# Optimization experiments

Hardware: AMD Instinct MI355X
Metric: run time of the kernel (lower is better)

The kernel has to match this reference:

```python
import jax, jax.numpy as jnp
import numpy as np

S, B, H, D, IN = 512, 8, 8, 64, 512  # seq, batch, heads, head dim, model dim
PROJ = H * (5 * D + 2)


def setup_inputs() -> dict:
    key = jax.random.key(0)
    k0, k1, k2 = jax.random.split(key, 3)
    x = jax.random.normal(k0, (S, B, IN), jnp.float32)
    W_slow = jax.random.normal(k1, (PROJ, IN), jnp.float32) / np.sqrt(IN).astype(np.float32)
    W_out = jax.random.normal(k2, (IN, H * D), jnp.float32) / np.sqrt(H * D).astype(np.float32)
    ln_gamma = jnp.ones((IN,), jnp.float32)
    ln_beta = jnp.zeros((IN,), jnp.float32)
    return dict(x=x, W_slow=W_slow, W_out=W_out, ln_gamma=ln_gamma, ln_beta=ln_beta)


def reference(x, W_slow, W_out, ln_gamma, ln_beta):
    slen, bsz, in_dim = x.shape
    # pre-LayerNorm (torch LayerNorm: biased variance, eps=1e-5)
    mu = x.mean(-1, keepdims=True)
    var = x.var(-1, keepdims=True)
    normed = (x - mu) / jnp.sqrt(var + 1e-5) * ln_gamma + ln_beta
    qkvb = (normed @ W_slow.T).reshape(slen, bsz, H, 5 * D + 2)
    q, k, v, rk, rv, beta, rbeta = jnp.split(
        qkvb, [D, 2 * D, 3 * D, 4 * D, 5 * D, 5 * D + 1], axis=-1)
    q = jax.nn.softmax(q, axis=-1)
    k = jax.nn.softmax(k, axis=-1)
    rk = jax.nn.softmax(rk, axis=-1)
    beta = jax.nn.sigmoid(beta)    # (S,B,H,1)
    rbeta = jax.nn.sigmoid(rbeta)  # (S,B,H,1)

    # ---- fast_weight_memory: delta-rule fast weight, z_t = W_t q_t ----
    W0 = jnp.zeros((bsz, H, D, D), x.dtype)

    def fw_step(W, inp):
        qt, kt, vt, bt = inp  # (B,H,D),(B,H,D),(B,H,D),(B,H,1)
        v_old = jnp.einsum('bhij,bhj->bhi', W, kt)
        W = W + (bt * (vt - v_old))[..., :, None] * kt[..., None, :]
        z = jnp.einsum('bhij,bhj->bhi', W, qt)
        return W, z

    _, z = jax.lax.scan(fw_step, W0, (q, k, v, beta))  # z: (S,B,H,D)

    # ---- fast_rnn_v2: recurrent fast weight, h_t = z_t + R_t softmax(h_{t-1}) ----
    R0 = jnp.zeros((bsz, H, D, D), x.dtype)
    h0 = jnp.zeros((bsz, H, D), x.dtype)

    def rec_step(carry, inp):
        R, h = carry
        zt, kt, vt, bt = inp
        qh = jax.nn.softmax(h, axis=-1)
        v_old = jnp.einsum('bhij,bhj->bhi', R, kt)
        R = R + (bt * (vt - v_old))[..., :, None] * kt[..., None, :]
        h = zt + jnp.einsum('bhij,bhj->bhi', R, qh)
        return (R, h), h

    _, hs = jax.lax.scan(rec_step, (R0, h0), (z, rk, rv, rbeta))  # (S,B,H,D)

    out = hs.reshape(slen, bsz, H * D) @ W_out.T  # (S,B,IN)
    # dropout = 0.0 -> identity; residual
    return x + out
```

## Files before the change

### kernel.cpp

```cpp
#include <hip/hip_runtime.h>

#define S_LEN 512
#define BSZ 8
#define NH 8
#define HD 64
#define IN_DIM 512
#define PROJ 2576
#define SEG 322
#define AST 352
#define CHUNK 8
#define NCH 64
#define CB (CHUNK * AST * 4)

typedef __attribute__((ext_vector_type(8))) __bf16 bf16x8;
typedef __attribute__((ext_vector_type(4))) float f32x4;

static __device__ __forceinline__ unsigned short f2bf(float f) {
  unsigned u = __float_as_uint(f);
  unsigned r = (u + 0x7fffu + ((u >> 16) & 1u)) >> 16;
  return (unsigned short)r;
}
static __device__ __forceinline__ float bf2f(unsigned short s) {
  return __uint_as_float(((unsigned)s) << 16);
}

static __device__ __forceinline__ void gl_lds16(const void* g, void* l) {
  __builtin_amdgcn_global_load_lds(
      (const __attribute__((address_space(1))) unsigned int*)g,
      (__attribute__((address_space(3))) unsigned int*)l, 16, 0, 0);
}

static __device__ __forceinline__ void barrier_lgkm() {
  asm volatile("s_waitcnt lgkmcnt(0)" ::: "memory");
  __builtin_amdgcn_s_barrier();
  asm volatile("" ::: "memory");
}

__global__ __launch_bounds__(256) void ln_kernel(const float* __restrict__ x,
                                                 const float* __restrict__ gamma,
                                                 const float* __restrict__ beta,
                                                 unsigned short* __restrict__ out) {
  int wave = threadIdx.x >> 6, lane = threadIdx.x & 63;
  int row = blockIdx.x * 4 + wave;
  const float* xr = x + (size_t)row * IN_DIM + lane * 8;
  float4 a = *(const float4*)xr;
  float4 b = *(const float4*)(xr + 4);
  float vals[8] = {a.x, a.y, a.z, a.w, b.x, b.y, b.z, b.w};
  float s = 0.f, ss = 0.f;
#pragma unroll
  for (int i = 0; i < 8; i++) { s += vals[i]; ss += vals[i] * vals[i]; }
#pragma unroll
  for (int o = 32; o; o >>= 1) { s += __shfl_xor(s, o); ss += __shfl_xor(ss, o); }
  float mu = s * (1.f / 512.f);
  float var = ss * (1.f / 512.f) - mu * mu;
  float rstd = rsqrtf(var + 1e-5f);
  const float* g = gamma + lane * 8;
  const float* be = beta + lane * 8;
  float4 g1 = *(const float4*)g, g2 = *(const float4*)(g + 4);
  float4 b1 = *(const float4*)be, b2 = *(const float4*)(be + 4);
  float gs[8] = {g1.x, g1.y, g1.z, g1.w, g2.x, g2.y, g2.z, g2.w};
  float bs[8] = {b1.x, b1.y, b1.z, b1.w, b2.x, b2.y, b2.z, b2.w};
  union { unsigned short u[8]; uint4 v; } pk;
#pragma unroll
  for (int i = 0; i < 8; i++) pk.u[i] = f2bf((vals[i] - mu) * rstd * gs[i] + bs[i]);
  *(uint4*)(out + (size_t)row * IN_DIM + lane * 8) = pk.v;
}

__global__ void cast_kernel(const float* __restrict__ in, unsigned short* __restrict__ out, int n) {
  int i = blockIdx.x * blockDim.x + threadIdx.x;
  int st = gridDim.x * blockDim.x;
  for (; i < n; i += st) out[i] = f2bf(in[i]);
}

template <int BF16_OUT, int RESID>
__global__ __launch_bounds__(256) void gemm_bt(const unsigned short* __restrict__ A,
                                               const unsigned short* __restrict__ B,
                                               void* __restrict__ Cout,
                                               const float* __restrict__ resid,
                                               int M, int N, int K) {
  __shared__ __align__(16) unsigned short As[64][40];
  __shared__ __align__(16) unsigned short Bs[64][40];
  int tid = threadIdx.x;
  int lane = tid & 63, wave = tid >> 6;
  int m0 = blockIdx.y * 64, n0 = blockIdx.x * 64;
  int srow = tid >> 2, skq = (tid & 3) * 8;
  const unsigned short* Ap = A + (size_t)(m0 + srow) * K + skq;
  const unsigned short* Bp = B + (size_t)(n0 + srow) * K + skq;
  bool bvalid = (n0 + srow) < N;
  f32x4 zero = {0.f, 0.f, 0.f, 0.f};
  f32x4 acc[4];
#pragma unroll
  for (int nt = 0; nt < 4; nt++) acc[nt] = zero;
  int q = lane >> 4, m16 = lane & 15;
  for (int k0 = 0; k0 < K; k0 += 32) {
    uint4 av = *(const uint4*)(Ap + k0);
    uint4 bz = {0u, 0u, 0u, 0u};
    uint4 bv = bvalid ? *(const uint4*)(Bp + k0) : bz;
    *(uint4*)&As[srow][skq] = av;
    *(uint4*)&Bs[srow][skq] = bv;
    __syncthreads();
    bf16x8 af = *(const bf16x8*)&As[wave * 16 + m16][q * 8];
#pragma unroll
    for (int nt = 0; nt < 4; nt++) {
      bf16x8 bfv = *(const bf16x8*)&Bs[nt * 16 + m16][q * 8];
      acc[nt] = __builtin_amdgcn_mfma_f32_16x16x32_bf16(af, bfv, acc[nt], 0, 0, 0);
    }
    __syncthreads();
  }
  int rbase = q * 4;
#pragma unroll
  for (int nt = 0; nt < 4; nt++) {
#pragma unroll
    for (int rr = 0; rr < 4; rr++) {
      int gm = m0 + wave * 16 + rbase + rr;
      int gn = n0 + nt * 16 + m16;
      if (gn < N) {
        float v = acc[nt][rr];
        if (BF16_OUT) {
          ((unsigned short*)Cout)[(size_t)gm * N + gn] = f2bf(v);
        } else {
          float o = v;
          if (RESID) o += resid[(size_t)gm * N + gn];
          ((float*)Cout)[(size_t)gm * N + gn] = o;
        }
      }
    }
  }
}

__global__ __launch_bounds__(256) void act_kernel(const unsigned short* __restrict__ qkvb,
                                                  float* __restrict__ act) {
  int gw = blockIdx.x * 4 + (threadIdx.x >> 6);
  int l = threadIdx.x & 63;
  int m = gw >> 3, hh = gw & 7;
  int t = m >> 3, b = m & 7;
  const unsigned short* src = qkvb + (size_t)m * PROJ + hh * SEG;
  float fq = bf2f(src[l]);
  float fk = bf2f(src[64 + l]);
  float fv = bf2f(src[128 + l]);
  float fr = bf2f(src[192 + l]);
  float frv = bf2f(src[256 + l]);
  float mq = fq, mk = fk, mr = fr;
#pragma unroll
  for (int o = 32; o; o >>= 1) {
    mq = fmaxf(mq, __shfl_xor(mq, o));
    mk = fmaxf(mk, __shfl_xor(mk, o));
    mr = fmaxf(mr, __shfl_xor(mr, o));
  }
  float eq = __expf(fq - mq), ek = __expf(fk - mk), er = __expf(fr - mr);
  float sq = eq, sk = ek, sr = er;
#pragma unroll
  for (int o = 32; o; o >>= 1) {
    sq += __shfl_xor(sq, o);
    sk += __shfl_xor(sk, o);
    sr += __shfl_xor(sr, o);
  }
  int bh = b * 8 + hh;
  float* dst = act + ((size_t)bh * S_LEN + t) * AST;
  dst[l] = eq * __builtin_amdgcn_rcpf(sq);
  dst[64 + l] = ek * __builtin_amdgcn_rcpf(sk);
  dst[128 + l] = er * __builtin_amdgcn_rcpf(sr);
  dst[192 + l] = fv;
  dst[256 + l] = frv;
  if (l < 2) {
    float xv = bf2f(src[320 + l]);
    dst[320 + l] = __builtin_amdgcn_rcpf(1.f + __expf(-xv));
  }
}

__global__ __launch_bounds__(128, 1) void scan_kernel(const float* __restrict__ act,
                                                      unsigned short* __restrict__ hs) {
  int bh = blockIdx.x;
  int b = bh >> 3, hh = bh & 7;
  int tid = threadIdx.x, l = tid & 63, w = tid >> 6;

  __shared__ __align__(16) float stage[2][CHUNK * AST];
  __shared__ __align__(16) float zbuf[2][64];
  __shared__ __align__(16) float ehb[64];

  const char* abase = (const char*)(act + (size_t)bh * S_LEN * AST);

#pragma unroll
  for (int i = 0; i < 6; i++) {
    int idx = i * 2 + w;
    if (idx < 11)
      gl_lds16(abase + (size_t)idx * 1024 + l * 16, (char*)&stage[0][0] + idx * 1024);
  }
  if (w) ehb[l] = 1.f;

  f32x4 M[16];
#pragma unroll
  for (int j = 0; j < 16; j++) M[j] = (f32x4){0.f, 0.f, 0.f, 0.f};

  unsigned short* hdst = hs + (size_t)b * 512 + hh * 64 + l;

  asm volatile("s_waitcnt vmcnt(0) lgkmcnt(0)" ::: "memory");
  __builtin_amdgcn_s_barrier();
  asm volatile("" ::: "memory");

  for (int c = 0; c < NCH; c++) {
    int buf = c & 1;
    if (c + 1 < NCH) {
      const char* nb = abase + (size_t)(c + 1) * CB;
#pragma unroll
      for (int i = 0; i < 6; i++) {
        int idx = i * 2 + w;
        if (idx < 11)
          gl_lds16(nb + (size_t)idx * 1024 + l * 16, (char*)&stage[buf ^ 1][0] + idx * 1024);
      }
    }

    for (int s = 0; s < CHUNK; s++) {
      const float* stf = &stage[buf][s * AST];
      const f32x4* st4 = (const f32x4*)stf;
      int p = s & 1;
      f32x4 z4 = {0.f, 0.f, 0.f, 0.f};

      if (w == 0) {
        float cv = stf[192 + l];
        f32x4 kk[16];
#pragma unroll
        for (int j = 0; j < 16; j++) kk[j] = st4[16 + j];
        f32x4 a0 = z4, a1 = z4, a2 = z4, a3 = z4;
#pragma unroll
        for (int j = 0; j < 16; j += 4) {
          a0 += M[j] * kk[j];
          a1 += M[j + 1] * kk[j + 1];
          a2 += M[j + 2] * kk[j + 2];
          a3 += M[j + 3] * kk[j + 3];
        }
        f32x4 vo = (a0 + a1) + (a2 + a3);
        float vold = (vo.x + vo.y) + (vo.z + vo.w);
        float bt = stf[320];
        float coef = bt * (cv - vold);
        f32x4 c4 = {coef, coef, coef, coef};
        a0 = a1 = a2 = a3 = z4;
#pragma unroll
        for (int j = 0; j < 16; j += 4) {
          M[j] += c4 * kk[j];         a0 += M[j] * st4[j];
          M[j + 1] += c4 * kk[j + 1]; a1 += M[j + 1] * st4[j + 1];
          M[j + 2] += c4 * kk[j + 2]; a2 += M[j + 2] * st4[j + 2];
          M[j + 3] += c4 * kk[j + 3]; a3 += M[j + 3] * st4[j + 3];
        }
        vo = (a0 + a1) + (a2 + a3);
        zbuf[p][l] = (vo.x + vo.y) + (vo.z + vo.w);
        barrier_lgkm();
      } else {
        float cv = stf[256 + l];
        f32x4 kk[16];
#pragma unroll
        for (int j = 0; j < 16; j++) kk[j] = st4[32 + j];
        f32x4 a0 = z4, a1 = z4, a2 = z4, a3 = z4;
#pragma unroll
        for (int j = 0; j < 16; j += 4) {
          a0 += M[j] * kk[j];
          a1 += M[j + 1] * kk[j + 1];
          a2 += M[j + 2] * kk[j + 2];
          a3 += M[j + 3] * kk[j + 3];
        }
        f32x4 vo = (a0 + a1) + (a2 + a3);
        float rvold = (vo.x + vo.y) + (vo.z + vo.w);
        float rb = stf[321];
        float coef = rb * (cv - rvold);
        f32x4 c4 = {coef, coef, coef, coef};
        const f32x4* e4 = (const f32x4*)ehb;
        f32x4 s0 = z4, s1 = z4, s2v = z4, s3 = z4;
        a0 = a1 = a2 = a3 = z4;
#pragma unroll
        for (int j = 0; j < 16; j += 4) {
          f32x4 e0 = e4[j], e1 = e4[j + 1], e2 = e4[j + 2], e3 = e4[j + 3];
          M[j] += c4 * kk[j];         a0 += M[j] * e0;       s0 += e0;
          M[j + 1] += c4 * kk[j + 1]; a1 += M[j + 1] * e1;   s1 += e1;
          M[j + 2] += c4 * kk[j + 2]; a2 += M[j + 2] * e2;   s2v += e2;
          M[j + 3] += c4 * kk[j + 3]; a3 += M[j + 3] * e3;   s3 += e3;
        }
        f32x4 ho = (a0 + a1) + (a2 + a3);
        f32x4 so = (s0 + s1) + (s2v + s3);
        float hp = (ho.x + ho.y) + (ho.z + ho.w);
        float sm = (so.x + so.y) + (so.z + so.w);
        barrier_lgkm();
        float z = zbuf[p][l];
        float h = z + hp * __builtin_amdgcn_rcpf(sm);
        hdst[(size_t)(c * CHUNK + s) * (BSZ * 512)] = f2bf(h);
        ehb[l] = __expf(h - 20.f);
      }
    }

    if (c + 1 < NCH) {
      if (w == 0) {
        asm volatile("s_waitcnt vmcnt(0)" ::: "memory");
      } else {
        asm volatile("s_waitcnt vmcnt(8)" ::: "memory");
      }
      __builtin_amdgcn_s_barrier();
      asm volatile("" ::: "memory");
    }
  }
}

extern "C" void kernel_launch(void* const* d_in, const int* in_sizes, int n_in,
                              void* d_out, int out_size, void* d_ws, size_t ws_size,
                              hipStream_t stream) {
  const float* x = (const float*)d_in[0];
  const float* W_slow = (const float*)d_in[1];
  const float* W_out = (const float*)d_in[2];
  const float* gamma = (const float*)d_in[3];
  const float* beta = (const float*)d_in[4];

  char* ws = (char*)d_ws;
  size_t off = 0;
  unsigned short* normed = (unsigned short*)(ws + off); off += (size_t)4096 * 512 * 2;
  unsigned short* Wslow_b = (unsigned short*)(ws + off); off += (size_t)PROJ * 512 * 2;
  unsigned short* Wout_b = (unsigned short*)(ws + off); off += (size_t)512 * 512 * 2;
  unsigned short* qkvb = (unsigned short*)(ws + off); off += (size_t)4096 * PROJ * 2;
  float* act = (float*)(ws + off); off += (size_t)64 * S_LEN * AST * 4;
  unsigned short* hsb = normed;

  hipLaunchKernelGGL(ln_kernel, dim3(1024), dim3(256), 0, stream, x, gamma, beta, normed);
  hipLaunchKernelGGL(cast_kernel, dim3(512), dim3(256), 0, stream, W_slow, Wslow_b, PROJ * 512);
  hipLaunchKernelGGL(cast_kernel, dim3(256), dim3(256), 0, stream, W_out, Wout_b, 512 * 512);
  hipLaunchKernelGGL((gemm_bt<1, 0>), dim3((PROJ + 63) / 64, 4096 / 64), dim3(256), 0, stream,
                     normed, Wslow_b, (void*)qkvb, (const float*)nullptr, 4096, PROJ, 512);
  hipLaunchKernelGGL(act_kernel, dim3(8192), dim3(256), 0, stream, qkvb, act);
  hipLaunchKernelGGL(scan_kernel, dim3(64), dim3(128), 0, stream, act, hsb);
  hipLaunchKernelGGL((gemm_bt<0, 1>), dim3(512 / 64, 4096 / 64), dim3(256), 0, stream,
                     hsb, Wout_b, d_out, x, 4096, 512, 512);
}
```

Baseline: 480.4 us.

## Fuse fast-weight matvecs via rank-1 identity and use packed FP32 FMAs

Each scan step now computes the old-state matvecs against the key and the query (or the softmax vector) together in one pass. The contribution of the rank-1 update is added algebraically as coef*(k·q), with the dot product built by a wave shuffle reduction. The M update is moved after the barrier, which takes it off the cross-wave critical path. Register math switches to v_pk_fma_f32 on float2 pairs, and the softmax normaliser is a shuffle sum instead of an LDS loop. The explicit initialisation of the shared ehb buffer was removed, so the first step multiplies the zero state by uninitialised LDS, and NaN or Inf values there could corrupt the output.

After: 586.7 us. 22.1% more time.

```diff
diff --git a/kernel.cpp b/kernel.cpp
--- a/kernel.cpp
+++ b/kernel.cpp
@@ -14,6 +14,9 @@
 
 typedef __attribute__((ext_vector_type(8))) __bf16 bf16x8;
 typedef __attribute__((ext_vector_type(4))) float f32x4;
+typedef __attribute__((ext_vector_type(2))) float f32x2;
+
+typedef union { f32x4 v4; f32x2 v2[2]; float f[4]; } u4;
 
 static __device__ __forceinline__ unsigned short f2bf(float f) {
   unsigned u = __float_as_uint(f);
@@ -22,6 +25,12 @@
 }
 static __device__ __forceinline__ float bf2f(unsigned short s) {
   return __uint_as_float(((unsigned)s) << 16);
+}
+
+static __device__ __forceinline__ f32x2 pk_fma(f32x2 a, f32x2 b, f32x2 c) {
+  f32x2 d;
+  asm("v_pk_fma_f32 %0, %1, %2, %3" : "=v"(d) : "v"(a), "v"(b), "v"(c));
+  return d;
 }
 
 static __device__ __forceinline__ void gl_lds16(const void* g, void* l) {
@@ -186,11 +195,11 @@
     if (idx < 11)
       gl_lds16(abase + (size_t)idx * 1024 + l * 16, (char*)&stage[0][0] + idx * 1024);
   }
-  if (w) ehb[l] = 1.f;
-
-  f32x4 M[16];
-#pragma unroll
-  for (int j = 0; j < 16; j++) M[j] = (f32x4){0.f, 0.f, 0.f, 0.f};
+
+  f32x2 M2[32];
+#pragma unroll
+  for (int j = 0; j < 32; j++) M2[j] = (f32x2){0.f, 0.f};
+  float ehl = 1.f;
 
   unsigned short* hdst = hs + (size_t)b * 512 + hh * 64 + l;
 
@@ -214,75 +223,88 @@
       const float* stf = &stage[buf][s * AST];
       const f32x4* st4 = (const f32x4*)stf;
       int p = s & 1;
-      f32x4 z4 = {0.f, 0.f, 0.f, 0.f};
+      f32x2 zr = {0.f, 0.f};
 
       if (w == 0) {
+        float kl = stf[64 + l], ql = stf[l];
+        float kq = kl * ql;
+#pragma unroll
+        for (int o = 32; o; o >>= 1) kq += __shfl_xor(kq, o);
         float cv = stf[192 + l];
-        f32x4 kk[16];
-#pragma unroll
-        for (int j = 0; j < 16; j++) kk[j] = st4[16 + j];
-        f32x4 a0 = z4, a1 = z4, a2 = z4, a3 = z4;
-#pragma unroll
-        for (int j = 0; j < 16; j += 4) {
-          a0 += M[j] * kk[j];
-          a1 += M[j + 1] * kk[j + 1];
-          a2 += M[j + 2] * kk[j + 2];
-          a3 += M[j + 3] * kk[j + 3];
+        float bt = stf[320];
+        f32x2 kk2[32];
+        f32x2 a0 = zr, a1 = zr, a2 = zr, a3 = zr;
+        f32x2 b0 = zr, b1 = zr, b2 = zr, b3 = zr;
+#pragma unroll
+        for (int j = 0; j < 16; j += 2) {
+          u4 kA; kA.v4 = st4[16 + j];
+          u4 kB; kB.v4 = st4[17 + j];
+          u4 qA; qA.v4 = st4[j];
+          u4 qB; qB.v4 = st4[j + 1];
+          kk2[2 * j] = kA.v2[0]; kk2[2 * j + 1] = kA.v2[1];
+          kk2[2 * j + 2] = kB.v2[0]; kk2[2 * j + 3] = kB.v2[1];
+          a0 = pk_fma(M2[2 * j], kA.v2[0], a0);
+          a1 = pk_fma(M2[2 * j + 1], kA.v2[1], a1);
+          a2 = pk_fma(M2[2 * j + 2], kB.v2[0], a2);
+          a3 = pk_fma(M2[2 * j + 3], kB.v2[1], a3);
+          b0 = pk_fma(M2[2 * j], qA.v2[0], b0);
+          b1 = pk_fma(M2[2 * j + 1], qA.v2[1], b1);
+          b2 = pk_fma(M2[2 * j + 2], qB.v2[0], b2);
+          b3 = pk_fma(M2[2 * j + 3], qB.v2[1], b3);
         }
-        f32x4 vo = (a0 + a1) + (a2 + a3);
-        float vold = (vo.x + vo.y) + (vo.z + vo.w);
-        float bt = stf[320];
+        f32x2 va = (a0 + a1) + (a2 + a3);
+        f32x2 vb = (b0 + b1) + (b2 + b3);
+        float vold = va.x + va.y;
+        float zq = vb.x + vb.y;
         float coef = bt * (cv - vold);
-        f32x4 c4 = {coef, coef, coef, coef};
-        a0 = a1 = a2 = a3 = z4;
-#pragma unroll
-        for (int j = 0; j < 16; j += 4) {
-          M[j] += c4 * kk[j];         a0 += M[j] * st4[j];
-          M[j + 1] += c4 * kk[j + 1]; a1 += M[j + 1] * st4[j + 1];
-          M[j + 2] += c4 * kk[j + 2]; a2 += M[j + 2] * st4[j + 2];
-          M[j + 3] += c4 * kk[j + 3]; a3 += M[j + 3] * st4[j + 3];
+        zbuf[p][l] = zq + coef * kq;
+        barrier_lgkm();
+        f32x2 c2 = {coef, coef};
+#pragma unroll
+        for (int j = 0; j < 32; j++) M2[j] = pk_fma(c2, kk2[j], M2[j]);
+      } else {
+        float rkl = stf[128 + l];
+        float pr = rkl * ehl, sm = ehl;
+#pragma unroll
+        for (int o = 32; o; o >>= 1) { pr += __shfl_xor(pr, o); sm += __shfl_xor(sm, o); }
+        float cv = stf[256 + l];
+        float rb = stf[321];
+        const f32x4* e4 = (const f32x4*)ehb;
+        f32x2 kk2[32];
+        f32x2 a0 = zr, a1 = zr, a2 = zr, a3 = zr;
+        f32x2 b0 = zr, b1 = zr, b2 = zr, b3 = zr;
+#pragma unroll
+        for (int j = 0; j < 16; j += 2) {
+          u4 kA; kA.v4 = st4[32 + j];
+          u4 kB; kB.v4 = st4[33 + j];
+          u4 eA; eA.v4 = e4[j];
+          u4 eB; eB.v4 = e4[j + 1];
+          kk2[2 * j] = kA.v2[0]; kk2[2 * j + 1] = kA.v2[1];
+          kk2[2 * j + 2] = kB.v2[0]; kk2[2 * j + 3] = kB.v2[1];
+          a0 = pk_fma(M2[2 * j], kA.v2[0], a0);
+          a1 = pk_fma(M2[2 * j + 1], kA.v2[1], a1);
+          a2 = pk_fma(M2[2 * j + 2], kB.v2[0], a2);
+          a3 = pk_fma(M2[2 * j + 3], kB.v2[1], a3);
+          b0 = pk_fma(M2[2 * j], eA.v2[0], b0);
+          b1 = pk_fma(M2[2 * j + 1], eA.v2[1], b1);
+          b2 = pk_fma(M2[2 * j + 2], eB.v2[0], b2);
+          b3 = pk_fma(M2[2 * j + 3], eB.v2[1], b3);
         }
-        vo = (a0 + a1) + (a2 + a3);
-        zbuf[p][l] = (vo.x + vo.y) + (vo.z + vo.w);
-        barrier_lgkm();
-      } else {
-        float cv = stf[256 + l];
-        f32x4 kk[16];
-#pragma unroll
-        for (int j = 0; j < 16; j++) kk[j] = st4[32 + j];
-        f32x4 a0 = z4, a1 = z4, a2 = z4, a3 = z4;
-#pragma unroll
-        for (int j = 0; j < 16; j += 4) {
-          a0 += M[j] * kk[j];
-          a1 += M[j + 1] * kk[j + 1];
-          a2 += M[j + 2] * kk[j + 2];
-          a3 += M[j + 3] * kk[j + 3];
-        }
-        f32x4 vo = (a0 + a1) + (a2 + a3);
-        float rvold = (vo.x + vo.y) + (vo.z + vo.w);
-        float rb = stf[321];
-        float coef = rb * (cv - rvold);
-        f32x4 c4 = {coef, coef, coef, coef};
-        const f32x4* e4 = (const f32x4*)ehb;
-        f32x4 s0 = z4, s1 = z4, s2v = z4, s3 = z4;
-        a0 = a1 = a2 = a3 = z4;
-#pragma unroll
-        for (int j = 0; j < 16; j += 4) {
-          f32x4 e0 = e4[j], e1 = e4[j + 1], e2 = e4[j + 2], e3 = e4[j + 3];
-          M[j] += c4 * kk[j];         a0 += M[j] * e0;       s0 += e0;
-          M[j + 1] += c4 * kk[j + 1]; a1 += M[j + 1] * e1;   s1 += e1;
-          M[j + 2] += c4 * kk[j + 2]; a2 += M[j + 2] * e2;   s2v += e2;
-          M[j + 3] += c4 * kk[j + 3]; a3 += M[j + 3] * e3;   s3 += e3;
-        }
-        f32x4 ho = (a0 + a1) + (a2 + a3);
-        f32x4 so = (s0 + s1) + (s2v + s3);
-        float hp = (ho.x + ho.y) + (ho.z + ho.w);
-        float sm = (so.x + so.y) + (so.z + so.w);
+        f32x2 va = (a0 + a1) + (a2 + a3);
+        f32x2 vb = (b0 + b1) + (b2 + b3);
+        float rvold = va.x + va.y;
+        float hpe = vb.x + vb.y;
+        float rcoef = rb * (cv - rvold);
+        float hp = hpe + rcoef * pr;
         barrier_lgkm();
         float z = zbuf[p][l];
+        f32x2 c2 = {rcoef, rcoef};
+#pragma unroll
+        for (int j = 0; j < 32; j++) M2[j] = pk_fma(c2, kk2[j], M2[j]);
         float h = z + hp * __builtin_amdgcn_rcpf(sm);
         hdst[(size_t)(c * CHUNK + s) * (BSZ * 512)] = f2bf(h);
-        ehb[l] = __expf(h - 20.f);
+        ehl = __expf(h - 20.f);
+        ehb[l] = ehl;
       }
     }
 
```

## Merge scan recurrences into one wave using packed FP32 FMAs

Applied to the files above, without the earlier changes.

The scan kernel previously split the two fast-weight recurrences across two waves and synchronized them with a block barrier and an LDS handoff of z at every time step. Now a single 64-lane wave holds both the W and R matrices in registers and runs both recurrences back to back. It uses v_pk_fma_f32 and v_pk_add_f32 to process two elements per instruction, which keeps the per-wave instruction count about the same as before. This removes the per-step barriers and the cross-wave z exchange. The cost is that the two recurrences now run serially within one wave, and register pressure rises to hold 128 floats of matrix state.

Measured after the change: 858.5 us. 1.79x slower.

```diff
diff --git a/kernel.cpp b/kernel.cpp
--- a/kernel.cpp
+++ b/kernel.cpp
@@ -14,6 +14,9 @@
 
 typedef __attribute__((ext_vector_type(8))) __bf16 bf16x8;
 typedef __attribute__((ext_vector_type(4))) float f32x4;
+typedef __attribute__((ext_vector_type(2))) float f32x2;
+
+typedef union { f32x4 v4; f32x2 v2[2]; float f[4]; } u4;
 
 static __device__ __forceinline__ unsigned short f2bf(float f) {
   unsigned u = __float_as_uint(f);
@@ -24,16 +27,21 @@
   return __uint_as_float(((unsigned)s) << 16);
 }
 
+static __device__ __forceinline__ f32x2 pk_fma(f32x2 a, f32x2 b, f32x2 c) {
+  f32x2 d;
+  asm("v_pk_fma_f32 %0, %1, %2, %3" : "=v"(d) : "v"(a), "v"(b), "v"(c));
+  return d;
+}
+static __device__ __forceinline__ f32x2 pk_add(f32x2 a, f32x2 b) {
+  f32x2 d;
+  asm("v_pk_add_f32 %0, %1, %2" : "=v"(d) : "v"(a), "v"(b));
+  return d;
+}
+
 static __device__ __forceinline__ void gl_lds16(const void* g, void* l) {
   __builtin_amdgcn_global_load_lds(
       (const __attribute__((address_space(1))) unsigned int*)g,
       (__attribute__((address_space(3))) unsigned int*)l, 16, 0, 0);
-}
-
-static __device__ __forceinline__ void barrier_lgkm() {
-  asm volatile("s_waitcnt lgkmcnt(0)" ::: "memory");
-  __builtin_amdgcn_s_barrier();
-  asm volatile("" ::: "memory");
 }
 
 __global__ __launch_bounds__(256) void ln_kernel(const float* __restrict__ x,
@@ -168,132 +176,128 @@
   }
 }
 
-__global__ __launch_bounds__(128, 1) void scan_kernel(const float* __restrict__ act,
-                                                      unsigned short* __restrict__ hs) {
+__global__ __launch_bounds__(64, 1) void scan_kernel(const float* __restrict__ act,
+                                                     unsigned short* __restrict__ hs) {
   int bh = blockIdx.x;
   int b = bh >> 3, hh = bh & 7;
-  int tid = threadIdx.x, l = tid & 63, w = tid >> 6;
+  int l = threadIdx.x;
 
   __shared__ __align__(16) float stage[2][CHUNK * AST];
-  __shared__ __align__(16) float zbuf[2][64];
   __shared__ __align__(16) float ehb[64];
 
   const char* abase = (const char*)(act + (size_t)bh * S_LEN * AST);
 
 #pragma unroll
-  for (int i = 0; i < 6; i++) {
-    int idx = i * 2 + w;
-    if (idx < 11)
-      gl_lds16(abase + (size_t)idx * 1024 + l * 16, (char*)&stage[0][0] + idx * 1024);
-  }
-  if (w) ehb[l] = 1.f;
-
-  f32x4 M[16];
-#pragma unroll
-  for (int j = 0; j < 16; j++) M[j] = (f32x4){0.f, 0.f, 0.f, 0.f};
+  for (int i = 0; i < 11; i++)
+    gl_lds16(abase + (size_t)i * 1024 + l * 16, (char*)&stage[0][0] + i * 1024);
+
+  f32x2 W2[32], R2[32];
+#pragma unroll
+  for (int j = 0; j < 32; j++) {
+    W2[j] = (f32x2){0.f, 0.f};
+    R2[j] = (f32x2){0.f, 0.f};
+  }
+  ehb[l] = 1.f;
 
   unsigned short* hdst = hs + (size_t)b * 512 + hh * 64 + l;
 
   asm volatile("s_waitcnt vmcnt(0) lgkmcnt(0)" ::: "memory");
-  __builtin_amdgcn_s_barrier();
-  asm volatile("" ::: "memory");
 
   for (int c = 0; c < NCH; c++) {
     int buf = c & 1;
     if (c + 1 < NCH) {
       const char* nb = abase + (size_t)(c + 1) * CB;
 #pragma unroll
-      for (int i = 0; i < 6; i++) {
-        int idx = i * 2 + w;
-        if (idx < 11)
-          gl_lds16(nb + (size_t)idx * 1024 + l * 16, (char*)&stage[buf ^ 1][0] + idx * 1024);
-      }
-    }
-
+      for (int i = 0; i < 11; i++)
+        gl_lds16(nb + (size_t)i * 1024 + l * 16, (char*)&stage[buf ^ 1][0] + i * 1024);
+    }
+
+#pragma unroll
     for (int s = 0; s < CHUNK; s++) {
       const float* stf = &stage[buf][s * AST];
       const f32x4* st4 = (const f32x4*)stf;
-      int p = s & 1;
-      f32x4 z4 = {0.f, 0.f, 0.f, 0.f};
-
-      if (w == 0) {
-        float cv = stf[192 + l];
-        f32x4 kk[16];
-#pragma unroll
-        for (int j = 0; j < 16; j++) kk[j] = st4[16 + j];
-        f32x4 a0 = z4, a1 = z4, a2 = z4, a3 = z4;
-#pragma unroll
-        for (int j = 0; j < 16; j += 4) {
-          a0 += M[j] * kk[j];
-          a1 += M[j + 1] * kk[j + 1];
-          a2 += M[j + 2] * kk[j + 2];
-          a3 += M[j + 3] * kk[j + 3];
-        }
-        f32x4 vo = (a0 + a1) + (a2 + a3);
-        float vold = (vo.x + vo.y) + (vo.z + vo.w);
-        float bt = stf[320];
-        float coef = bt * (cv - vold);
-        f32x4 c4 = {coef, coef, coef, coef};
-        a0 = a1 = a2 = a3 = z4;
-#pragma unroll
-        for (int j = 0; j < 16; j += 4) {
-          M[j] += c4 * kk[j];         a0 += M[j] * st4[j];
-          M[j + 1] += c4 * kk[j + 1]; a1 += M[j + 1] * st4[j + 1];
-          M[j + 2] += c4 * kk[j + 2]; a2 += M[j + 2] * st4[j + 2];
-          M[j + 3] += c4 * kk[j + 3]; a3 += M[j + 3] * st4[j + 3];
-        }
-        vo = (a0 + a1) + (a2 + a3);
-        zbuf[p][l] = (vo.x + vo.y) + (vo.z + vo.w);
-        barrier_lgkm();
-      } else {
-        float cv = stf[256 + l];
-        f32x4 kk[16];
-#pragma unroll
-        for (int j = 0; j < 16; j++) kk[j] = st4[32 + j];
-        f32x4 a0 = z4, a1 = z4, a2 = z4, a3 = z4;
-#pragma unroll
-        for (int j = 0; j < 16; j += 4) {
-          a0 += M[j] * kk[j];
-          a1 += M[j + 1] * kk[j + 1];
-          a2 += M[j + 2] * kk[j + 2];
-          a3 += M[j + 3] * kk[j + 3];
-        }
-        f32x4 vo = (a0 + a1) + (a2 + a3);
-        float rvold = (vo.x + vo.y) + (vo.z + vo.w);
-        float rb = stf[321];
-        float coef = rb * (cv - rvold);
-        f32x4 c4 = {coef, coef, coef, coef};
-        const f32x4* e4 = (const f32x4*)ehb;
-        f32x4 s0 = z4, s1 = z4, s2v = z4, s3 = z4;
-        a0 = a1 = a2 = a3 = z4;
-#pragma unroll
-        for (int j = 0; j < 16; j += 4) {
-          f32x4 e0 = e4[j], e1 = e4[j + 1], e2 = e4[j + 2], e3 = e4[j + 3];
-          M[j] += c4 * kk[j];         a0 += M[j] * e0;       s0 += e0;
-          M[j + 1] += c4 * kk[j + 1]; a1 += M[j + 1] * e1;   s1 += e1;
-          M[j + 2] += c4 * kk[j + 2]; a2 += M[j + 2] * e2;   s2v += e2;
-          M[j + 3] += c4 * kk[j + 3]; a3 += M[j + 3] * e3;   s3 += e3;
-        }
-        f32x4 ho = (a0 + a1) + (a2 + a3);
-        f32x4 so = (s0 + s1) + (s2v + s3);
-        float hp = (ho.x + ho.y) + (ho.z + ho.w);
-        float sm = (so.x + so.y) + (so.z + so.w);
-        barrier_lgkm();
-        float z = zbuf[p][l];
-        float h = z + hp * __builtin_amdgcn_rcpf(sm);
-        hdst[(size_t)(c * CHUNK + s) * (BSZ * 512)] = f2bf(h);
-        ehb[l] = __expf(h - 20.f);
-      }
+      const f32x2 zz = {0.f, 0.f};
+
+      u4 kv[16];
+      f32x2 a0 = zz, a1 = zz, a2 = zz, a3 = zz;
+#pragma unroll
+      for (int j = 0; j < 16; j += 2) {
+        kv[j].v4 = st4[16 + j];
+        kv[j + 1].v4 = st4[17 + j];
+        a0 = pk_fma(W2[2 * j], kv[j].v2[0], a0);
+        a1 = pk_fma(W2[2 * j + 1], kv[j].v2[1], a1);
+        a2 = pk_fma(W2[2 * j + 2], kv[j + 1].v2[0], a2);
+        a3 = pk_fma(W2[2 * j + 3], kv[j + 1].v2[1], a3);
+      }
+      f32x2 vo = pk_add(pk_add(a0, a1), pk_add(a2, a3));
+      float vold = vo.x + vo.y;
+      float cv = stf[192 + l];
+      float coef = stf[320] * (cv - vold);
+      f32x2 c2 = {coef, coef};
+      a0 = zz; a1 = zz; a2 = zz; a3 = zz;
+#pragma unroll
+      for (int j = 0; j < 16; j += 2) {
+        u4 qA, qB;
+        qA.v4 = st4[j];
+        qB.v4 = st4[j + 1];
+        W2[2 * j] = pk_fma(c2, kv[j].v2[0], W2[2 * j]);
+        a0 = pk_fma(W2[2 * j], qA.v2[0], a0);
+        W2[2 * j + 1] = pk_fma(c2, kv[j].v2[1], W2[2 * j + 1]);
+        a1 = pk_fma(W2[2 * j + 1], qA.v2[1], a1);
+        W2[2 * j + 2] = pk_fma(c2, kv[j + 1].v2[0], W2[2 * j + 2]);
+        a2 = pk_fma(W2[2 * j + 2], qB.v2[0], a2);
+        W2[2 * j + 3] = pk_fma(c2, kv[j + 1].v2[1], W2[2 * j + 3]);
+        a3 = pk_fma(W2[2 * j + 3], qB.v2[1], a3);
+      }
+      vo = pk_add(pk_add(a0, a1), pk_add(a2, a3));
+      float z = vo.x + vo.y;
+
+      f32x2 b0 = zz, b1 = zz, b2 = zz, b3 = zz;
+#pragma unroll
+      for (int j = 0; j < 16; j += 2) {
+        kv[j].v4 = st4[32 + j];
+        kv[j + 1].v4 = st4[33 + j];
+        b0 = pk_fma(R2[2 * j], kv[j].v2[0], b0);
+        b1 = pk_fma(R2[2 * j + 1], kv[j].v2[1], b1);
+        b2 = pk_fma(R2[2 * j + 2], kv[j + 1].v2[0], b2);
+        b3 = pk_fma(R2[2 * j + 3], kv[j + 1].v2[1], b3);
+      }
+      f32x2 ro = pk_add(pk_add(b0, b1), pk_add(b2, b3));
+      float rvold = ro.x + ro.y;
+      float rcv = stf[256 + l];
+      float rcoef = stf[321] * (rcv - rvold);
+      f32x2 rc2 = {rcoef, rcoef};
+      const f32x4* e4 = (const f32x4*)ehb;
+      f32x2 s0 = zz, s1 = zz;
+      b0 = zz; b1 = zz; b2 = zz; b3 = zz;
+#pragma unroll
+      for (int j = 0; j < 16; j += 2) {
+        u4 eA, eB;
+        eA.v4 = e4[j];
+        eB.v4 = e4[j + 1];
+        R2[2 * j] = pk_fma(rc2, kv[j].v2[0], R2[2 * j]);
+        b0 = pk_fma(R2[2 * j], eA.v2[0], b0);
+        R2[2 * j + 1] = pk_fma(rc2, kv[j].v2[1], R2[2 * j + 1]);
+        b1 = pk_fma(R2[2 * j + 1], eA.v2[1], b1);
+        R2[2 * j + 2] = pk_fma(rc2, kv[j + 1].v2[0], R2[2 * j + 2]);
+        b2 = pk_fma(R2[2 * j + 2], eB.v2[0], b2);
+        R2[2 * j + 3] = pk_fma(rc2, kv[j + 1].v2[1], R2[2 * j + 3]);
+        b3 = pk_fma(R2[2 * j + 3], eB.v2[1], b3);
+        s0 = pk_add(s0, pk_add(eA.v2[0], eA.v2[1]));
+        s1 = pk_add(s1, pk_add(eB.v2[0], eB.v2[1]));
+      }
+      ro = pk_add(pk_add(b0, b1), pk_add(b2, b3));
+      float hp = ro.x + ro.y;
+      f32x2 sv = pk_add(s0, s1);
+      float sm = sv.x + sv.y;
+
+      float h = z + hp * __builtin_amdgcn_rcpf(sm);
+      hdst[(size_t)(c * CHUNK + s) * (BSZ * 512)] = f2bf(h);
+      ehb[l] = __expf(h - 20.f);
     }
 
     if (c + 1 < NCH) {
-      if (w == 0) {
-        asm volatile("s_waitcnt vmcnt(0)" ::: "memory");
-      } else {
-        asm volatile("s_waitcnt vmcnt(8)" ::: "memory");
-      }
-      __builtin_amdgcn_s_barrier();
-      asm volatile("" ::: "memory");
+      asm volatile("s_waitcnt vmcnt(8)" ::: "memory");
     }
   }
 }
@@ -322,7 +326,7 @@
   hipLaunchKernelGGL((gemm_bt<1, 0>), dim3((PROJ + 63) / 64, 4096 / 64), dim3(256), 0, stream,
                      normed, Wslow_b, (void*)qkvb, (const float*)nullptr, 4096, PROJ, 512);
   hipLaunchKernelGGL(act_kernel, dim3(8192), dim3(256), 0, stream, qkvb, act);
-  hipLaunchKernelGGL(scan_kernel, dim3(64), dim3(128), 0, stream, act, hsb);
+  hipLaunchKernelGGL(scan_kernel, dim3(64), dim3(64), 0, stream, act, hsb);
   hipLaunchKernelGGL((gemm_bt<0, 1>), dim3(512 / 64, 4096 / 64), dim3(256), 0, stream,
                      hsb, Wout_b, d_out, x, 4096, 512, 512);
 }
```

## Decouple scan waves with LDS flag producer-consumer pipeline instead of per-step barriers

Applied to the files above, without the earlier changes.

Before, the two waves of the scan kernel shared a block barrier on every timestep. Now wave 0 (the delta-rule memory) runs ahead as a producer. It writes z for a whole chunk into a 4-deep LDS ring and publishes progress through a volatile LDS flag, while wave 1 (the recurrent fast weight) spins on that flag per chunk. Wave 0 alone issues the staging loads into a 4-buffer ring and waits on wave 1's progress flag before reusing a buffer. The intent is to remove the per-step barrier so the two serial recurrences overlap, at the cost of spin-wait correctness risk and more LDS.

Result: faster. 404.3 us (-15.8%).

```diff
diff --git a/kernel.cpp b/kernel.cpp
--- a/kernel.cpp
+++ b/kernel.cpp
@@ -28,12 +28,6 @@
   __builtin_amdgcn_global_load_lds(
       (const __attribute__((address_space(1))) unsigned int*)g,
       (__attribute__((address_space(3))) unsigned int*)l, 16, 0, 0);
-}
-
-static __device__ __forceinline__ void barrier_lgkm() {
-  asm volatile("s_waitcnt lgkmcnt(0)" ::: "memory");
-  __builtin_amdgcn_s_barrier();
-  asm volatile("" ::: "memory");
 }
 
 __global__ __launch_bounds__(256) void ln_kernel(const float* __restrict__ x,
@@ -174,49 +168,51 @@
   int b = bh >> 3, hh = bh & 7;
   int tid = threadIdx.x, l = tid & 63, w = tid >> 6;
 
-  __shared__ __align__(16) float stage[2][CHUNK * AST];
-  __shared__ __align__(16) float zbuf[2][64];
+  __shared__ __align__(16) float stage[4][CHUNK * AST];
+  __shared__ __align__(16) float zring[4][CHUNK][64];
   __shared__ __align__(16) float ehb[64];
+  __shared__ int flags[16];
+
+  volatile int* w0done = &flags[0];
+  volatile int* w1done = &flags[8];
 
   const char* abase = (const char*)(act + (size_t)bh * S_LEN * AST);
 
-#pragma unroll
-  for (int i = 0; i < 6; i++) {
-    int idx = i * 2 + w;
-    if (idx < 11)
-      gl_lds16(abase + (size_t)idx * 1024 + l * 16, (char*)&stage[0][0] + idx * 1024);
-  }
+  if (tid == 0) { flags[0] = 0; flags[8] = 0; }
   if (w) ehb[l] = 1.f;
+  if (w == 0) {
+#pragma unroll
+    for (int i = 0; i < 11; i++)
+      gl_lds16(abase + (size_t)i * 1024 + l * 16, (char*)&stage[0][0] + i * 1024);
+  }
+  __syncthreads();
 
   f32x4 M[16];
 #pragma unroll
   for (int j = 0; j < 16; j++) M[j] = (f32x4){0.f, 0.f, 0.f, 0.f};
-
-  unsigned short* hdst = hs + (size_t)b * 512 + hh * 64 + l;
-
-  asm volatile("s_waitcnt vmcnt(0) lgkmcnt(0)" ::: "memory");
-  __builtin_amdgcn_s_barrier();
-  asm volatile("" ::: "memory");
-
-  for (int c = 0; c < NCH; c++) {
-    int buf = c & 1;
-    if (c + 1 < NCH) {
-      const char* nb = abase + (size_t)(c + 1) * CB;
-#pragma unroll
-      for (int i = 0; i < 6; i++) {
-        int idx = i * 2 + w;
-        if (idx < 11)
-          gl_lds16(nb + (size_t)idx * 1024 + l * 16, (char*)&stage[buf ^ 1][0] + idx * 1024);
-      }
-    }
-
-    for (int s = 0; s < CHUNK; s++) {
-      const float* stf = &stage[buf][s * AST];
-      const f32x4* st4 = (const f32x4*)stf;
-      int p = s & 1;
-      f32x4 z4 = {0.f, 0.f, 0.f, 0.f};
-
-      if (w == 0) {
+  const f32x4 z4 = {0.f, 0.f, 0.f, 0.f};
+
+  if (w == 0) {
+    for (int c = 0; c < NCH; c++) {
+      if (c >= 3) {
+        while (*w1done < c - 2) __builtin_amdgcn_s_sleep(2);
+      }
+      if (c + 1 < NCH) {
+        const char* nb = abase + (size_t)(c + 1) * CB;
+        char* sb = (char*)&stage[(c + 1) & 3][0];
+#pragma unroll
+        for (int i = 0; i < 11; i++)
+          gl_lds16(nb + (size_t)i * 1024 + l * 16, sb + i * 1024);
+        asm volatile("s_waitcnt vmcnt(11)" ::: "memory");
+      } else {
+        asm volatile("s_waitcnt vmcnt(0)" ::: "memory");
+      }
+      const float* cb = &stage[c & 3][0];
+      float* zc = &zring[c & 3][0][0];
+#pragma unroll
+      for (int s = 0; s < CHUNK; s++) {
+        const float* stf = cb + s * AST;
+        const f32x4* st4 = (const f32x4*)stf;
         float cv = stf[192 + l];
         f32x4 kk[16];
 #pragma unroll
@@ -243,9 +239,22 @@
           M[j + 3] += c4 * kk[j + 3]; a3 += M[j + 3] * st4[j + 3];
         }
         vo = (a0 + a1) + (a2 + a3);
-        zbuf[p][l] = (vo.x + vo.y) + (vo.z + vo.w);
-        barrier_lgkm();
-      } else {
+        zc[s * 64 + l] = (vo.x + vo.y) + (vo.z + vo.w);
+      }
+      asm volatile("s_waitcnt lgkmcnt(0)" ::: "memory");
+      *w0done = c + 1;
+    }
+  } else {
+    unsigned short* hdst = hs + (size_t)b * 512 + hh * 64 + l;
+    for (int c = 0; c < NCH; c++) {
+      while (*w0done < c + 1) __builtin_amdgcn_s_sleep(2);
+      const float* cb = &stage[c & 3][0];
+      const float* zc = &zring[c & 3][0][0];
+#pragma unroll
+      for (int s = 0; s < CHUNK; s++) {
+        const float* stf = cb + s * AST;
+        const f32x4* st4 = (const f32x4*)stf;
+        float z = zc[s * 64 + l];
         float cv = stf[256 + l];
         f32x4 kk[16];
 #pragma unroll
@@ -261,8 +270,8 @@
         f32x4 vo = (a0 + a1) + (a2 + a3);
         float rvold = (vo.x + vo.y) + (vo.z + vo.w);
         float rb = stf[321];
-        float coef = rb * (cv - rvold);
-        f32x4 c4 = {coef, coef, coef, coef};
+        float rcoef = rb * (cv - rvold);
+        f32x4 c4 = {rcoef, rcoef, rcoef, rcoef};
         const f32x4* e4 = (const f32x4*)ehb;
         f32x4 s0 = z4, s1 = z4, s2v = z4, s3 = z4;
         a0 = a1 = a2 = a3 = z4;
@@ -278,22 +287,12 @@
         f32x4 so = (s0 + s1) + (s2v + s3);
         float hp = (ho.x + ho.y) + (ho.z + ho.w);
         float sm = (so.x + so.y) + (so.z + so.w);
-        barrier_lgkm();
-        float z = zbuf[p][l];
         float h = z + hp * __builtin_amdgcn_rcpf(sm);
         hdst[(size_t)(c * CHUNK + s) * (BSZ * 512)] = f2bf(h);
         ehb[l] = __expf(h - 20.f);
       }
-    }
-
-    if (c + 1 < NCH) {
-      if (w == 0) {
-        asm volatile("s_waitcnt vmcnt(0)" ::: "memory");
-      } else {
-        asm volatile("s_waitcnt vmcnt(8)" ::: "memory");
-      }
-      __builtin_amdgcn_s_barrier();
-      asm volatile("" ::: "memory");
+      asm volatile("s_waitcnt lgkmcnt(0)" ::: "memory");
+      *w1done = c + 1;
     }
   }
 }
```
